# Optimization experiments

Measured on AMD Instinct MI355X. Metric: run time of the kernel, lower is better.

The kernel has to match this reference:

```python
import jax, jax.numpy as jnp
import numpy as np

TAU = 2.0      # LIF membrane time constant
ALPHA = 4.0    # spikingjelly surrogate.Sigmoid default alpha
EPS = 1e-5     # BatchNorm eps
HEADS = 8

@jax.custom_vjp
def heaviside(x):
    return (x >= 0).astype(x.dtype)

def _hv_fwd(x):
    return (x >= 0).astype(x.dtype), x

def _hv_bwd(x, g):
    s = jax.nn.sigmoid(ALPHA * x)
    return (g * ALPHA * s * (1.0 - s),)

heaviside.defvjp(_hv_fwd, _hv_bwd)

def lif(x, vth=1.0):
    # multi-step LIF, decay_input=True, v_reset=0 (hard reset), detach_reset=True
    def step(v, xt):
        v = v + (xt - v) / TAU
        s = heaviside(v - vth)
        v = v * (1.0 - jax.lax.stop_gradient(s))
        return v, s
    _, spikes = jax.lax.scan(step, jnp.zeros_like(x[0]), x)
    return spikes

def bn(x, gamma, beta, mean, var):
    # x: [T,B,C,N]; eval-mode BatchNorm1d over channel axis 2
    inv = gamma * jax.lax.rsqrt(var + EPS)
    return x * inv[None, None, :, None] + (beta - mean * inv)[None, None, :, None]

def conv1x1(x, w):
    # x: [T,B,C,N], w: [Cout,Cin] (Conv1d kernel_size=1)
    return jnp.einsum('tbcn,dc->tbdn', x, w)

def setup_inputs():
    key = jax.random.key(0)
    ks = jax.random.split(key, 24)
    T, B, C, H, W = 4, 16, 512, 32, 32
    scale = 1.0 / np.sqrt(C)
    d = {}
    d['x'] = jax.random.normal(ks[0], (T, B, C, H, W), jnp.float32)
    def bn_params(i):
        g = 1.0 + 0.1 * jax.random.normal(ks[i], (C,), jnp.float32)
        b = 0.1 * jax.random.normal(ks[i + 1], (C,), jnp.float32)
        m = 0.1 * jax.random.normal(ks[i + 2], (C,), jnp.float32)
        v = jax.random.uniform(ks[i + 3], (C,), jnp.float32, 0.5, 1.5)
        return g, b, m, v
    d['q_w'] = scale * jax.random.normal(ks[1], (C, C), jnp.float32)
    d['q_gamma'], d['q_beta'], d['q_mean'], d['q_var'] = bn_params(2)
    d['k_w'] = scale * jax.random.normal(ks[6], (C, C), jnp.float32)
    d['k_gamma'], d['k_beta'], d['k_mean'], d['k_var'] = bn_params(7)
    d['proj_w'] = scale * jax.random.normal(ks[11], (C, C), jnp.float32)
    d['proj_b'] = 0.01 * jax.random.normal(ks[12], (C,), jnp.float32)
    d['p_gamma'], d['p_beta'], d['p_mean'], d['p_var'] = bn_params(13)
    return d

def reference(x, q_w, q_gamma, q_beta, q_mean, q_var,
              k_w, k_gamma, k_beta, k_mean, k_var,
              proj_w, proj_b, p_gamma, p_beta, p_mean, p_var):
    T, B, C, H, W = x.shape
    N = H * W
    Dh = C // HEADS
    xs = lif(x).reshape(T, B, C, N)                    # shortcut_lif then flatten(3)
    q = lif(bn(conv1x1(xs, q_w), q_gamma, q_beta, q_mean, q_var))
    k = lif(bn(conv1x1(xs, k_w), k_gamma, k_beta, k_mean, k_var))
    qh = q.reshape(T, B, HEADS, Dh, N).sum(axis=3, keepdims=True)  # [T,B,h,1,N]
    attn = lif(qh, vth=0.5)
    kh = k.reshape(T, B, HEADS, Dh, N)
    y = (attn * kh).reshape(T, B, C, N)
    y = bn(conv1x1(y, proj_w) + proj_b[None, None, :, None],
           p_gamma, p_beta, p_mean, p_var)
    return y.reshape(T, B, C, H, W), attn
```

## Files before the change

### kernel.cpp

```cpp
#include <hip/hip_runtime.h>

typedef unsigned short u16;
typedef unsigned int u32;
typedef float f32x4 __attribute__((ext_vector_type(4)));
typedef short s16x8 __attribute__((ext_vector_type(8)));

#define T_ 4
#define B_ 16
#define C_ 512
#define N_ 1024
#define YSZ 33554432

__device__ __forceinline__ u16 f2bf(float f) {
  u32 u = __float_as_uint(f);
  u32 r = u + 0x7FFFu + ((u >> 16) & 1u);
  return (u16)(r >> 16);
}
__device__ __forceinline__ float bf2f(u16 h) { return __uint_as_float(((u32)h) << 16); }

__device__ __forceinline__ void async16(const void* g, void* l) {
  __builtin_amdgcn_global_load_lds((const __attribute__((address_space(1))) void*)g,
                                   (__attribute__((address_space(3))) void*)l, 16, 0, 0);
}

__global__ void prep_kernel(const float* __restrict__ qw, const float* __restrict__ kw,
                            const float* __restrict__ pw,
                            const float* __restrict__ qg, const float* __restrict__ qb,
                            const float* __restrict__ qm, const float* __restrict__ qv,
                            const float* __restrict__ kg, const float* __restrict__ kb,
                            const float* __restrict__ km, const float* __restrict__ kv,
                            const float* __restrict__ pg, const float* __restrict__ pbt,
                            const float* __restrict__ pm, const float* __restrict__ pv,
                            u16* __restrict__ whlq, u16* __restrict__ whlk,
                            u16* __restrict__ pwb, float* __restrict__ consts) {
  int blk = blockIdx.x, tid = threadIdx.x;
  if (blk < 512) {
    int d = blk;
    for (int c = tid; c < 512; c += 256) {
      float w = qw[d * 512 + c];
      u16 hi = f2bf(w);
      whlq[d * 1024 + c] = hi;
      whlq[d * 1024 + 512 + c] = f2bf(w - bf2f(hi));
      w = kw[d * 512 + c];
      hi = f2bf(w);
      whlk[d * 1024 + c] = hi;
      whlk[d * 1024 + 512 + c] = f2bf(w - bf2f(hi));
      pwb[d * 512 + c] = f2bf(pw[d * 512 + c]);
    }
  } else {
    for (int c = tid; c < 512; c += 256) {
      float inv = qg[c] / sqrtf(qv[c] + 1e-5f);
      consts[c] = inv; consts[512 + c] = qb[c] - qm[c] * inv;
      inv = kg[c] / sqrtf(kv[c] + 1e-5f);
      consts[1024 + c] = inv; consts[1536 + c] = kb[c] - km[c] * inv;
      inv = pg[c] / sqrtf(pv[c] + 1e-5f);
      consts[2048 + c] = inv; consts[2560 + c] = pbt[c] - pm[c] * inv;
    }
  }
}

__global__ __launch_bounds__(256) void lifx_kernel(const float* __restrict__ x,
                                                   u16* __restrict__ xs) {
  int b = blockIdx.z;
  int cbase = blockIdx.y * 64, nbase = blockIdx.x * 64;
  int tid = threadIdx.x;
  int c_l = tid >> 6, n_l = tid & 63;
  __shared__ __align__(16) u16 tile[64 * 72];
  float v[16];
#pragma unroll
  for (int i = 0; i < 16; ++i) v[i] = 0.f;
  for (int t = 0; t < 4; ++t) {
    const float* xp = x + ((size_t)(t * 16 + b) * 512 + cbase + c_l * 16) * 1024 + nbase + n_l;
#pragma unroll
    for (int i = 0; i < 16; ++i) {
      float xv = xp[(size_t)i * 1024];
      float vn = v[i] + 0.5f * (xv - v[i]);
      bool s = vn >= 1.0f;
      tile[n_l * 72 + c_l * 16 + i] = s ? 0x3F80 : 0;
      v[i] = s ? 0.f : vn;
    }
    __syncthreads();
    u16* yb = xs + ((size_t)(t * 16 + b) * 1024 + nbase) * 512 + cbase;
#pragma unroll
    for (int e = 0; e < 2; ++e) {
      int chunk = tid * 2 + e;
      int n = chunk >> 3, c0 = (chunk & 7) * 8;
      *(uint4*)&yb[(size_t)n * 512 + c0] = *(const uint4*)&tile[n * 72 + c0];
    }
    __syncthreads();
  }
}

__global__ __launch_bounds__(512, 2) void gemm_qk_kernel(
    const u16* __restrict__ Aq, const u16* __restrict__ Ak,
    const u16* __restrict__ Bbase, const float* __restrict__ consts,
    float* __restrict__ dout, u16* __restrict__ y) {
  const int tid = threadIdx.x;
  const int lane = tid & 63, w = tid >> 6;
  const bool isQ = w < 4;
  const int rw = isQ ? w : (w - 4);
  const int wm = rw >> 1, wn = rw & 1;
  const int quad = lane >> 4, l16 = lane & 15;
  const int b = blockIdx.z;
  const int m_blk = blockIdx.y * 128, n_blk = blockIdx.x * 128;
  const int srow = lane >> 3;
  const int scol = (((lane & 7) ^ srow) & 7) * 8;
  __shared__ __align__(16) u16 smem[40960];
  u16* Aqh = smem;
  u16* Aql = smem + 8192;
  u16* Akh = smem + 16384;
  u16* Akl = smem + 24576;
  u16* Bs  = smem + 32768;
  float* attn_s = (float*)(smem + 32768);
  u16* Ys = smem;
  u16* Ah = isQ ? Aqh : Akh;
  u16* Al = isQ ? Aql : Akl;
  const int cb = isQ ? 0 : 1024;
  const int rxor = l16 & 7;
  float v[64];
#pragma unroll
  for (int i = 0; i < 64; ++i) v[i] = 0.f;
  float va[4] = {0.f, 0.f, 0.f, 0.f};

  for (int t = 0; t < 4; ++t) {
    f32x4 acc[4][4];
    const f32x4 zero = {0.f, 0.f, 0.f, 0.f};
#pragma unroll
    for (int i = 0; i < 4; ++i)
#pragma unroll
      for (int j = 0; j < 4; ++j) acc[i][j] = zero;
    const u16* Bt = Bbase + (size_t)(t * 16 + b) * (N_ * C_);

    for (int k0 = 0; k0 < 512; k0 += 64) {
#pragma unroll
      for (int j = 0; j < 2; ++j) {
        int r = j * 64 + w * 8 + srow;
        int lo = (j * 64 + w * 8) * 64;
        const size_t ar = (size_t)(m_blk + r) * 1024 + k0 + scol;
        async16(Aq + ar,       &Aqh[lo]);
        async16(Aq + ar + 512, &Aql[lo]);
        async16(Ak + ar,       &Akh[lo]);
        async16(Ak + ar + 512, &Akl[lo]);
        async16(Bt + (size_t)(n_blk + r) * 512 + k0 + scol, &Bs[lo]);
      }
      __syncthreads();
#pragma unroll
      for (int kk = 0; kk < 2; ++kk) {
        s16x8 ah[4], al[4], bf[4];
        const int slot = ((kk * 4 + quad) ^ rxor) * 8;
#pragma unroll
        for (int ti = 0; ti < 4; ++ti) {
          ah[ti] = *(const s16x8*)&Ah[(wm * 64 + ti * 16 + l16) * 64 + slot];
          al[ti] = *(const s16x8*)&Al[(wm * 64 + ti * 16 + l16) * 64 + slot];
        }
#pragma unroll
        for (int tj = 0; tj < 4; ++tj)
          bf[tj] = *(const s16x8*)&Bs[(wn * 64 + tj * 16 + l16) * 64 + slot];
#pragma unroll
        for (int ti = 0; ti < 4; ++ti)
#pragma unroll
          for (int tj = 0; tj < 4; ++tj) {
            acc[ti][tj] = __builtin_amdgcn_mfma_f32_16x16x32_bf16(ah[ti], bf[tj], acc[ti][tj], 0, 0, 0);
            acc[ti][tj] = __builtin_amdgcn_mfma_f32_16x16x32_bf16(al[ti], bf[tj], acc[ti][tj], 0, 0, 0);
          }
      }
      __syncthreads();
    }

    if (isQ) {
      float qp[4] = {0.f, 0.f, 0.f, 0.f};
#pragma unroll
      for (int ti = 0; ti < 4; ++ti) {
#pragma unroll
        for (int r = 0; r < 4; ++r) {
          int row = m_blk + wm * 64 + ti * 16 + quad * 4 + r;
          float iv = consts[row], ib = consts[512 + row];
#pragma unroll
          for (int tj = 0; tj < 4; ++tj) {
            float bnv = acc[ti][tj][r] * iv + ib;
            float vv = v[(ti * 4 + tj) * 4 + r];
            float vn = vv + 0.5f * (bnv - vv);
            bool s = vn >= 1.0f;
            v[(ti * 4 + tj) * 4 + r] = s ? 0.f : vn;
            qp[tj] += s ? 1.f : 0.f;
          }
        }
      }
      int h = (m_blk >> 6) + wm;
#pragma unroll
      for (int tj = 0; tj < 4; ++tj) {
        float q = qp[tj];
        q += __shfl_xor(q, 16, 64);
        q += __shfl_xor(q, 32, 64);
        float vn = va[tj] + 0.5f * (q - va[tj]);
        bool s = vn >= 0.5f;
        va[tj] = s ? 0.f : vn;
        if (quad == 0) {
          int cl = wn * 64 + tj * 16 + l16;
          float sv = s ? 1.f : 0.f;
          attn_s[wm * 128 + cl] = sv;
          dout[(size_t)YSZ + ((size_t)(t * 16 + b) * 8 + h) * 1024 + n_blk + cl] = sv;
        }
      }
    }
    __syncthreads();

    if (!isQ) {
      float at[4];
#pragma unroll
      for (int tj = 0; tj < 4; ++tj)
        at[tj] = attn_s[wm * 128 + wn * 64 + tj * 16 + l16];
#pragma unroll
      for (int ti = 0; ti < 4; ++ti) {
        u16 pk[4][4];
#pragma unroll
        for (int r = 0; r < 4; ++r) {
          int row = m_blk + wm * 64 + ti * 16 + quad * 4 + r;
          float iv = consts[cb + row], ib = consts[cb + 512 + row];
#pragma unroll
          for (int tj = 0; tj < 4; ++tj) {
            float bnv = acc[ti][tj][r] * iv + ib;
            float vv = v[(ti * 4 + tj) * 4 + r];
            float vn = vv + 0.5f * (bnv - vv);
            bool s = vn >= 1.0f;
            v[(ti * 4 + tj) * 4 + r] = s ? 0.f : vn;
            pk[tj][r] = (s && at[tj] != 0.f) ? 0x3F80 : 0;
          }
        }
#pragma unroll
        for (int tj = 0; tj < 4; ++tj) {
          int n_loc = wn * 64 + tj * 16 + l16;
          int c_loc = wm * 64 + ti * 16 + quad * 4;
          u32 lo2 = (u32)pk[tj][0] | ((u32)pk[tj][1] << 16);
          u32 hi2 = (u32)pk[tj][2] | ((u32)pk[tj][3] << 16);
          uint2 pv2; pv2.x = lo2; pv2.y = hi2;
          *(uint2*)&Ys[n_loc * 132 + c_loc] = pv2;
        }
      }
    }
    __syncthreads();
    u16* yb = y + ((size_t)(t * 16 + b) * 1024 + n_blk) * 512 + m_blk;
#pragma unroll
    for (int p = 0; p < 4; ++p) {
      int idx = p * 512 + tid;
      int rown = idx >> 4, ch = (idx & 15) * 8;
      *(uint4*)&yb[(size_t)rown * 512 + ch] = *(const uint4*)&Ys[rown * 132 + ch];
    }
    __syncthreads();
  }
}

__global__ __launch_bounds__(256, 3) void gemm_proj_kernel(
    const u16* __restrict__ A, const u16* __restrict__ Bbase,
    float* __restrict__ outP, const float* __restrict__ projb,
    const float* __restrict__ consts) {
  const int tid = threadIdx.x;
  const int lane = tid & 63, w = tid >> 6;
  const int wm = w >> 1, wn = w & 1;
  const int quad = lane >> 4, l16 = lane & 15;
  const int tb = blockIdx.z;
  const int m_blk = blockIdx.y * 128, n_blk = blockIdx.x * 128;
  const int srow = lane >> 3;
  const int scol = (((lane & 7) ^ srow) & 7) * 8;
  __shared__ __align__(16) u16 As[128 * 64];
  __shared__ __align__(16) u16 Bs[128 * 64];
  f32x4 acc[4][4];
  const f32x4 zero = {0.f, 0.f, 0.f, 0.f};
#pragma unroll
  for (int i = 0; i < 4; ++i)
#pragma unroll
    for (int j = 0; j < 4; ++j) acc[i][j] = zero;
  const u16* Bt = Bbase + (size_t)tb * (N_ * C_);
  const int rxor = l16 & 7;

  for (int k0 = 0; k0 < 512; k0 += 64) {
#pragma unroll
    for (int i = 0; i < 4; ++i) {
      int r = i * 32 + w * 8 + srow;
      async16(A + (size_t)(m_blk + r) * 512 + k0 + scol, &As[(i * 32 + w * 8) * 64]);
      async16(Bt + (size_t)(n_blk + r) * 512 + k0 + scol, &Bs[(i * 32 + w * 8) * 64]);
    }
    __syncthreads();
#pragma unroll
    for (int kk = 0; kk < 2; ++kk) {
      s16x8 af[4], bf[4];
      const int slot = ((kk * 4 + quad) ^ rxor) * 8;
#pragma unroll
      for (int ti = 0; ti < 4; ++ti)
        af[ti] = *(const s16x8*)&As[(wm * 64 + ti * 16 + l16) * 64 + slot];
#pragma unroll
      for (int tj = 0; tj < 4; ++tj)
        bf[tj] = *(const s16x8*)&Bs[(wn * 64 + tj * 16 + l16) * 64 + slot];
#pragma unroll
      for (int ti = 0; ti < 4; ++ti)
#pragma unroll
        for (int tj = 0; tj < 4; ++tj)
          acc[ti][tj] = __builtin_amdgcn_mfma_f32_16x16x32_bf16(af[ti], bf[tj], acc[ti][tj], 0, 0, 0);
    }
    __syncthreads();
  }

  const float* pinv = consts + 2048;
  const float* pb2 = consts + 2560;
  float* o = outP + (size_t)tb * (C_ * N_);
#pragma unroll
  for (int ti = 0; ti < 4; ++ti) {
    int row0 = m_blk + wm * 64 + ti * 16 + quad * 4;
#pragma unroll
    for (int r = 0; r < 4; ++r) {
      int row = row0 + r;
      float bi = projb[row], piv = pinv[row], pbi = pb2[row];
#pragma unroll
      for (int tj = 0; tj < 4; ++tj) {
        int col = n_blk + wn * 64 + tj * 16 + l16;
        o[(size_t)row * N_ + col] = (acc[ti][tj][r] + bi) * piv + pbi;
      }
    }
  }
}

extern "C" void kernel_launch(void* const* d_in, const int* in_sizes, int n_in,
                              void* d_out, int out_size, void* d_ws, size_t ws_size,
                              hipStream_t stream) {
  const float* x   = (const float*)d_in[0];
  const float* qw  = (const float*)d_in[1];
  const float* qg  = (const float*)d_in[2];
  const float* qb  = (const float*)d_in[3];
  const float* qm  = (const float*)d_in[4];
  const float* qv  = (const float*)d_in[5];
  const float* kw  = (const float*)d_in[6];
  const float* kg  = (const float*)d_in[7];
  const float* kb  = (const float*)d_in[8];
  const float* km  = (const float*)d_in[9];
  const float* kv  = (const float*)d_in[10];
  const float* pw  = (const float*)d_in[11];
  const float* pb  = (const float*)d_in[12];
  const float* pg  = (const float*)d_in[13];
  const float* pbt = (const float*)d_in[14];
  const float* pm  = (const float*)d_in[15];
  const float* pv  = (const float*)d_in[16];
  float* out = (float*)d_out;
  char* ws = (char*)d_ws;

  u16* xs       = (u16*)ws;
  u16* y2       = (u16*)(ws + 67108864);
  u16* whlq     = (u16*)(ws + 201326592);
  u16* whlk     = (u16*)(ws + 202375168);
  u16* pwb      = (u16*)(ws + 203423744);
  float* consts = (float*)(ws + 203948032);

  prep_kernel<<<513, 256, 0, stream>>>(qw, kw, pw, qg, qb, qm, qv, kg, kb, km, kv,
                                       pg, pbt, pm, pv, whlq, whlk, pwb, consts);
  lifx_kernel<<<dim3(16, 8, 16), 256, 0, stream>>>(x, xs);
  gemm_qk_kernel<<<dim3(8, 4, 16), 512, 0, stream>>>(whlq, whlk, xs, consts, out, y2);
  gemm_proj_kernel<<<dim3(8, 4, 64), 256, 0, stream>>>(pwb, y2, out, pb, consts);
}
```

Measured before the change: 467.7 us.

## Split Q and K GEMMs into separate blocks, apply attention mask in projection GEMM

Q and K LIF GEMMs used to run in one 512-thread block, each half of the warps holding its own A tiles. Now they run as separate 256-thread blocks, giving twice the grid and a smaller LDS footprint. The attention spike mask, which needed Q results inside the K block, is no longer applied when writing y2. Instead the projection GEMM reads the attention output from global memory and zeroes B fragments per head. This relies on each 64-wide K step of the projection matching exactly one head. It also adds a global attention read per K step and an ordering dependency on the Q blocks having written attention before the projection kernel runs, which the stream order guarantees.

```diff
diff --git a/kernel.cpp b/kernel.cpp
--- a/kernel.cpp
+++ b/kernel.cpp
@@ -91,31 +91,27 @@
   }
 }
 
-__global__ __launch_bounds__(512, 2) void gemm_qk_kernel(
+__global__ __launch_bounds__(256, 2) void gemm_qk_kernel(
     const u16* __restrict__ Aq, const u16* __restrict__ Ak,
     const u16* __restrict__ Bbase, const float* __restrict__ consts,
     float* __restrict__ dout, u16* __restrict__ y) {
   const int tid = threadIdx.x;
   const int lane = tid & 63, w = tid >> 6;
-  const bool isQ = w < 4;
-  const int rw = isQ ? w : (w - 4);
-  const int wm = rw >> 1, wn = rw & 1;
+  const int wm = w >> 1, wn = w & 1;
   const int quad = lane >> 4, l16 = lane & 15;
-  const int b = blockIdx.z;
+  const int z = blockIdx.z;
+  const int b = z & 15;
+  const bool isK = z >= 16;
   const int m_blk = blockIdx.y * 128, n_blk = blockIdx.x * 128;
   const int srow = lane >> 3;
   const int scol = (((lane & 7) ^ srow) & 7) * 8;
-  __shared__ __align__(16) u16 smem[40960];
-  u16* Aqh = smem;
-  u16* Aql = smem + 8192;
-  u16* Akh = smem + 16384;
-  u16* Akl = smem + 24576;
-  u16* Bs  = smem + 32768;
-  float* attn_s = (float*)(smem + 32768);
-  u16* Ys = smem;
-  u16* Ah = isQ ? Aqh : Akh;
-  u16* Al = isQ ? Aql : Akl;
-  const int cb = isQ ? 0 : 1024;
+  __shared__ __align__(16) u16 smem[3 * 128 * 64];
+  u16* Ash = smem;
+  u16* Asl = smem + 8192;
+  u16* Bs  = smem + 16384;
+  u16* Ys  = smem;
+  const u16* A = isK ? Ak : Aq;
+  const int cb = isK ? 1024 : 0;
   const int rxor = l16 & 7;
   float v[64];
 #pragma unroll
@@ -133,14 +129,11 @@
 
     for (int k0 = 0; k0 < 512; k0 += 64) {
 #pragma unroll
-      for (int j = 0; j < 2; ++j) {
-        int r = j * 64 + w * 8 + srow;
-        int lo = (j * 64 + w * 8) * 64;
-        const size_t ar = (size_t)(m_blk + r) * 1024 + k0 + scol;
-        async16(Aq + ar,       &Aqh[lo]);
-        async16(Aq + ar + 512, &Aql[lo]);
-        async16(Ak + ar,       &Akh[lo]);
-        async16(Ak + ar + 512, &Akl[lo]);
+      for (int i = 0; i < 4; ++i) {
+        int r = i * 32 + w * 8 + srow;
+        int lo = (i * 32 + w * 8) * 64;
+        async16(A + (size_t)(m_blk + r) * 1024 + k0 + scol, &Ash[lo]);
+        async16(A + (size_t)(m_blk + r) * 1024 + 512 + k0 + scol, &Asl[lo]);
         async16(Bt + (size_t)(n_blk + r) * 512 + k0 + scol, &Bs[lo]);
       }
       __syncthreads();
@@ -150,8 +143,8 @@
         const int slot = ((kk * 4 + quad) ^ rxor) * 8;
 #pragma unroll
         for (int ti = 0; ti < 4; ++ti) {
-          ah[ti] = *(const s16x8*)&Ah[(wm * 64 + ti * 16 + l16) * 64 + slot];
-          al[ti] = *(const s16x8*)&Al[(wm * 64 + ti * 16 + l16) * 64 + slot];
+          ah[ti] = *(const s16x8*)&Ash[(wm * 64 + ti * 16 + l16) * 64 + slot];
+          al[ti] = *(const s16x8*)&Asl[(wm * 64 + ti * 16 + l16) * 64 + slot];
         }
 #pragma unroll
         for (int tj = 0; tj < 4; ++tj)
@@ -167,7 +160,7 @@
       __syncthreads();
     }
 
-    if (isQ) {
+    if (!isK) {
       float qp[4] = {0.f, 0.f, 0.f, 0.f};
 #pragma unroll
       for (int ti = 0; ti < 4; ++ti) {
@@ -196,20 +189,11 @@
         bool s = vn >= 0.5f;
         va[tj] = s ? 0.f : vn;
         if (quad == 0) {
-          int cl = wn * 64 + tj * 16 + l16;
-          float sv = s ? 1.f : 0.f;
-          attn_s[wm * 128 + cl] = sv;
-          dout[(size_t)YSZ + ((size_t)(t * 16 + b) * 8 + h) * 1024 + n_blk + cl] = sv;
-        }
-      }
-    }
-    __syncthreads();
-
-    if (!isQ) {
-      float at[4];
-#pragma unroll
-      for (int tj = 0; tj < 4; ++tj)
-        at[tj] = attn_s[wm * 128 + wn * 64 + tj * 16 + l16];
+          int col = n_blk + wn * 64 + tj * 16 + l16;
+          dout[(size_t)YSZ + ((size_t)(t * 16 + b) * 8 + h) * 1024 + col] = s ? 1.f : 0.f;
+        }
+      }
+    } else {
 #pragma unroll
       for (int ti = 0; ti < 4; ++ti) {
         u16 pk[4][4];
@@ -224,7 +208,7 @@
             float vn = vv + 0.5f * (bnv - vv);
             bool s = vn >= 1.0f;
             v[(ti * 4 + tj) * 4 + r] = s ? 0.f : vn;
-            pk[tj][r] = (s && at[tj] != 0.f) ? 0x3F80 : 0;
+            pk[tj][r] = s ? 0x3F80 : 0;
           }
         }
 #pragma unroll
@@ -237,23 +221,23 @@
           *(uint2*)&Ys[n_loc * 132 + c_loc] = pv2;
         }
       }
-    }
-    __syncthreads();
-    u16* yb = y + ((size_t)(t * 16 + b) * 1024 + n_blk) * 512 + m_blk;
-#pragma unroll
-    for (int p = 0; p < 4; ++p) {
-      int idx = p * 512 + tid;
-      int rown = idx >> 4, ch = (idx & 15) * 8;
-      *(uint4*)&yb[(size_t)rown * 512 + ch] = *(const uint4*)&Ys[rown * 132 + ch];
-    }
-    __syncthreads();
+      __syncthreads();
+      u16* yb = y + ((size_t)(t * 16 + b) * 1024 + n_blk) * 512 + m_blk;
+#pragma unroll
+      for (int p = 0; p < 8; ++p) {
+        int idx = p * 256 + tid;
+        int rown = idx >> 4, ch = (idx & 15) * 8;
+        *(uint4*)&yb[(size_t)rown * 512 + ch] = *(const uint4*)&Ys[rown * 132 + ch];
+      }
+      __syncthreads();
+    }
   }
 }
 
 __global__ __launch_bounds__(256, 3) void gemm_proj_kernel(
     const u16* __restrict__ A, const u16* __restrict__ Bbase,
     float* __restrict__ outP, const float* __restrict__ projb,
-    const float* __restrict__ consts) {
+    const float* __restrict__ consts, const float* __restrict__ attn) {
   const int tid = threadIdx.x;
   const int lane = tid & 63, w = tid >> 6;
   const int wm = w >> 1, wn = w & 1;
@@ -266,11 +250,13 @@
   __shared__ __align__(16) u16 Bs[128 * 64];
   f32x4 acc[4][4];
   const f32x4 zero = {0.f, 0.f, 0.f, 0.f};
+  const s16x8 zero8 = {0, 0, 0, 0, 0, 0, 0, 0};
 #pragma unroll
   for (int i = 0; i < 4; ++i)
 #pragma unroll
     for (int j = 0; j < 4; ++j) acc[i][j] = zero;
   const u16* Bt = Bbase + (size_t)tb * (N_ * C_);
+  const float* attn_tb = attn + (size_t)tb * 8192;
   const int rxor = l16 & 7;
 
   for (int k0 = 0; k0 < 512; k0 += 64) {
@@ -280,6 +266,11 @@
       async16(A + (size_t)(m_blk + r) * 512 + k0 + scol, &As[(i * 32 + w * 8) * 64]);
       async16(Bt + (size_t)(n_blk + r) * 512 + k0 + scol, &Bs[(i * 32 + w * 8) * 64]);
     }
+    const int h = k0 >> 6;
+    float atf[4];
+#pragma unroll
+    for (int tj = 0; tj < 4; ++tj)
+      atf[tj] = attn_tb[h * 1024 + n_blk + wn * 64 + tj * 16 + l16];
     __syncthreads();
 #pragma unroll
     for (int kk = 0; kk < 2; ++kk) {
@@ -289,8 +280,10 @@
       for (int ti = 0; ti < 4; ++ti)
         af[ti] = *(const s16x8*)&As[(wm * 64 + ti * 16 + l16) * 64 + slot];
 #pragma unroll
-      for (int tj = 0; tj < 4; ++tj)
+      for (int tj = 0; tj < 4; ++tj) {
         bf[tj] = *(const s16x8*)&Bs[(wn * 64 + tj * 16 + l16) * 64 + slot];
+        bf[tj] = (atf[tj] != 0.f) ? bf[tj] : zero8;
+      }
 #pragma unroll
       for (int ti = 0; ti < 4; ++ti)
 #pragma unroll
@@ -352,6 +345,7 @@
   prep_kernel<<<513, 256, 0, stream>>>(qw, kw, pw, qg, qb, qm, qv, kg, kb, km, kv,
                                        pg, pbt, pm, pv, whlq, whlk, pwb, consts);
   lifx_kernel<<<dim3(16, 8, 16), 256, 0, stream>>>(x, xs);
-  gemm_qk_kernel<<<dim3(8, 4, 16), 512, 0, stream>>>(whlq, whlk, xs, consts, out, y2);
-  gemm_proj_kernel<<<dim3(8, 4, 64), 256, 0, stream>>>(pwb, y2, out, pb, consts);
-}
+  gemm_qk_kernel<<<dim3(8, 4, 32), 256, 0, stream>>>(whlq, whlk, xs, consts, out, y2);
+  gemm_proj_kernel<<<dim3(8, 4, 64), 256, 0, stream>>>(pwb, y2, out, pb, consts,
+                                                       out + YSZ);
+}
```

After: 452.9 us. 1.03x faster.
